# Kernel tuning notes

Measured on AMD Instinct MI355X. Metric: run time of the kernel, lower is better.

Reference implementation:

```python
import jax, jax.numpy as jnp
import numpy as np
import math

INPUT_DIM = 1024
EMBED_DIM = 1024
NUM_HEADS = 16
HEAD_DIM = EMBED_DIM // NUM_HEADS


def setup_inputs() -> dict:
    key = jax.random.key(0)
    k_x, k_qkv, k_out_w, k_out_b = jax.random.split(key, 4)
    x = jax.random.normal(k_x, (1, 4096, INPUT_DIM), dtype=jnp.float32)
    # nn.Linear weights are [out, in]; kaiming-uniform-ish scale
    s1 = 1.0 / math.sqrt(INPUT_DIM)
    s2 = 1.0 / math.sqrt(EMBED_DIM)
    qkv_w = jax.random.uniform(k_qkv, (3 * EMBED_DIM, INPUT_DIM), jnp.float32, -s1, s1)
    out_w = jax.random.uniform(k_out_w, (EMBED_DIM, EMBED_DIM), jnp.float32, -s2, s2)
    out_b = jax.random.uniform(k_out_b, (EMBED_DIM,), jnp.float32, -s2, s2)
    return {"x": x, "qkv_w": qkv_w, "out_w": out_w, "out_b": out_b}


def reference(x, qkv_w, out_w, out_b):
    B, N, C = x.shape
    qkv = jnp.einsum('bnc,ec->bne', x, qkv_w)  # [B,N,3E]
    q = qkv[:, :, 0:EMBED_DIM].reshape(B, N, NUM_HEADS, HEAD_DIM)
    k = qkv[:, :, EMBED_DIM:2 * EMBED_DIM].reshape(B, N, NUM_HEADS, HEAD_DIM)
    v = qkv[:, :, 2 * EMBED_DIM:].reshape(B, N, NUM_HEADS, HEAD_DIM)
    scores = jnp.einsum('bihd,bjhd->bhij', q, k) / jnp.sqrt(jnp.float32(HEAD_DIM))
    attn = jax.nn.softmax(scores, axis=-1)  # [B,H,N,N]
    out = jnp.einsum('bhik,bkhd->bhid', attn, v)
    out = out.transpose(0, 2, 1, 3).reshape(B, N, EMBED_DIM)
    return jnp.einsum('bne,fe->bnf', out, out_w) + out_b
```

## Files before the change

### kernel.cpp

```cpp
#include <hip/hip_runtime.h>
#include <hip/hip_bf16.h>

typedef __bf16 bf16;
typedef bf16 bf16x8 __attribute__((ext_vector_type(8)));
typedef bf16 bf16x4 __attribute__((ext_vector_type(4)));
typedef float f32x4 __attribute__((ext_vector_type(4)));

#define MFMA16(a, b, c) __builtin_amdgcn_mfma_f32_16x16x32_bf16(a, b, c, 0, 0, 0)

__device__ __forceinline__ void g2l16(const bf16* g, bf16* l) {
  __builtin_amdgcn_global_load_lds(
      (__attribute__((address_space(1))) void*)(void*)g,
      (__attribute__((address_space(3))) void*)l,
      16, 0, 0);
}

__device__ __forceinline__ int sniff_inblock(const void* x, int tid) {
  __shared__ int sf;
  if (tid < 64) {
    unsigned short v = ((const unsigned short*)x)[tid];
    int e = (v >> 7) & 0xFF;
    int sane = (e == 0) || (e >= 112 && e <= 142);
    unsigned long long m = __ballot(sane);
    if (tid == 0) sf = (__popcll(m) >= 56) ? 1 : 0;
  }
  __syncthreads();
  return sf;
}

__device__ __forceinline__ void conv8(const void* in, bf16* out, long i, int f) {
  if (f) {
    ((bf16x8*)out)[i] = ((const bf16x8*)in)[i];
  } else {
    const float4* p = (const float4*)in;
    float4 a = p[i * 2], b = p[i * 2 + 1];
    bf16x8 v;
    v[0] = (bf16)a.x; v[1] = (bf16)a.y; v[2] = (bf16)a.z; v[3] = (bf16)a.w;
    v[4] = (bf16)b.x; v[5] = (bf16)b.y; v[6] = (bf16)b.z; v[7] = (bf16)b.w;
    ((bf16x8*)out)[i] = v;
  }
}

__global__ void convert2_to_bf16(const void* __restrict__ a, bf16* __restrict__ oa,
                                 long na8, const void* __restrict__ b,
                                 bf16* __restrict__ ob, long nb8,
                                 const void* __restrict__ x) {
  const int f = sniff_inblock(x, threadIdx.x);
  long i = (long)blockIdx.x * 256 + threadIdx.x;
  if (i < na8) conv8(a, oa, i, f);
  else if (i - na8 < nb8) conv8(b, ob, i - na8, f);
}

__global__ __launch_bounds__(256) void gemm_qkv(
    const bf16* __restrict__ A, const bf16* __restrict__ B,
    bf16* __restrict__ qB, bf16* __restrict__ kP, bf16* __restrict__ vP) {
  __shared__ __align__(16) bf16 As[128 * 32];
  __shared__ __align__(16) bf16 Bs[128 * 32];

  const int tid  = threadIdx.x;
  const int lane = tid & 63;
  const int wave = tid >> 6;
  const int wm   = wave >> 1, wn = wave & 1;
  const int l15  = lane & 15, quad = lane >> 4;
  const long m0 = (long)blockIdx.x * 128;
  const long n0 = (long)blockIdx.y * 128;
  const int  K  = 1024;

  const bf16* Ab = A + m0 * K;
  const bf16* Bb = B + n0 * K;
  const int rowA = tid & 127;
  const int dc   = tid >> 7;

  f32x4 acc[4][4] = {};

  for (int k0 = 0; k0 < K; k0 += 32) {
    g2l16(Ab + (long)rowA * K + k0 + dc * 8,       As + tid * 8);
    g2l16(Ab + (long)rowA * K + k0 + (dc + 2) * 8, As + (tid + 256) * 8);
    g2l16(Bb + (long)rowA * K + k0 + dc * 8,       Bs + tid * 8);
    g2l16(Bb + (long)rowA * K + k0 + (dc + 2) * 8, Bs + (tid + 256) * 8);
    __syncthreads();

    bf16x8 af[4], bfr[4];
#pragma unroll
    for (int t = 0; t < 4; t++) {
      af[t]  = *(const bf16x8*)(As + (quad * 128 + wm * 64 + t * 16 + l15) * 8);
      bfr[t] = *(const bf16x8*)(Bs + (quad * 128 + wn * 64 + t * 16 + l15) * 8);
    }
#pragma unroll
    for (int tm = 0; tm < 4; tm++)
#pragma unroll
      for (int tn = 0; tn < 4; tn++)
        acc[tm][tn] = MFMA16(af[tm], bfr[tn], acc[tm][tn]);
    __syncthreads();
  }

  const long rb = m0 + wm * 64;
  const long cb = n0 + wn * 64;
  const int third = (int)(n0 >> 10);
  const float QSC = 0.125f * 1.44269504088896f;

#pragma unroll
  for (int tm = 0; tm < 4; tm++) {
#pragma unroll
    for (int tn = 0; tn < 4; tn++) {
      const long r0 = rb + tm * 16 + quad * 4;
      const long c  = cb + tn * 16 + l15;
      if (third == 0) {
#pragma unroll
        for (int r = 0; r < 4; r++)
          qB[(r0 + r) * 1024 + c] = (bf16)(acc[tm][tn][r] * QSC);
      } else if (third == 1) {
        const int ep = (int)c - 1024;
        const int h = ep >> 6, d = ep & 63;
        const int n0r = (int)r0;
        const int kt = n0r >> 6;
        const int kh = (n0r >> 5) & 1;
        const int t_ = (n0r >> 2) & 1;
        const int mq = (n0r >> 3) & 3;
        const long base = ((long)h * 64 + kt) * 4096 +
                          (((d >> 3) * 64) + kh * 32 + t_ * 16 + mq * 4) * 8 +
                          (d & 7);
#pragma unroll
        for (int r = 0; r < 4; r++)
          kP[base + r * 8] = (bf16)acc[tm][tn][r];
      } else {
        const int ep = (int)c - 2048;
        const int h = ep >> 6, d = ep & 63;
        const int n0r = (int)r0;
        const int kt = n0r >> 6;
        const int kh = (n0r >> 5) & 1;
        const int kq = (n0r >> 3) & 3;
        bf16x4 v;
#pragma unroll
        for (int r = 0; r < 4; r++) v[r] = (bf16)acc[tm][tn][r];
        *(bf16x4*)(vP + ((long)h * 64 + kt) * 4096 +
                   (kh * 256 + kq * 64 + d) * 8 + (quad & 1) * 4) = v;
      }
    }
  }
}

template <bool BIAS, bool DYNOUT>
__global__ __launch_bounds__(256) void gemm_bt(
    const bf16* __restrict__ A, const bf16* __restrict__ B,
    void* __restrict__ Cv, const bf16* __restrict__ bias,
    int M, int Nn, int K, const void* __restrict__ xs) {
  __shared__ __align__(16) bf16 As[128 * 32];
  __shared__ __align__(16) bf16 Bs[128 * 32];

  const int tid  = threadIdx.x;
  const int obf = DYNOUT ? sniff_inblock(xs, tid) : 1;

  const int lane = tid & 63;
  const int wave = tid >> 6;
  const int wm   = wave >> 1, wn = wave & 1;
  const int l15  = lane & 15, quad = lane >> 4;
  const long m0 = (long)blockIdx.x * 128;
  const long n0 = (long)blockIdx.y * 128;

  const bf16* Ab = A + m0 * K;
  const bf16* Bb = B + n0 * K;
  const int rowA = tid & 127;
  const int dc   = tid >> 7;

  f32x4 acc[4][4] = {};

  for (int k0 = 0; k0 < K; k0 += 32) {
    g2l16(Ab + (long)rowA * K + k0 + dc * 8,       As + tid * 8);
    g2l16(Ab + (long)rowA * K + k0 + (dc + 2) * 8, As + (tid + 256) * 8);
    g2l16(Bb + (long)rowA * K + k0 + dc * 8,       Bs + tid * 8);
    g2l16(Bb + (long)rowA * K + k0 + (dc + 2) * 8, Bs + (tid + 256) * 8);
    __syncthreads();

    bf16x8 af[4], bfr[4];
#pragma unroll
    for (int t = 0; t < 4; t++) {
      af[t]  = *(const bf16x8*)(As + (quad * 128 + wm * 64 + t * 16 + l15) * 8);
      bfr[t] = *(const bf16x8*)(Bs + (quad * 128 + wn * 64 + t * 16 + l15) * 8);
    }
#pragma unroll
    for (int tm = 0; tm < 4; tm++)
#pragma unroll
      for (int tn = 0; tn < 4; tn++)
        acc[tm][tn] = MFMA16(af[tm], bfr[tn], acc[tm][tn]);
    __syncthreads();
  }

  const long rb = m0 + wm * 64;
  const long cb = n0 + wn * 64;
#pragma unroll
  for (int tm = 0; tm < 4; tm++) {
#pragma unroll
    for (int tn = 0; tn < 4; tn++) {
      const long r0 = rb + tm * 16 + quad * 4;
      const long c  = cb + tn * 16 + l15;
      const float bv = BIAS ? (float)bias[c] : 0.0f;
#pragma unroll
      for (int r = 0; r < 4; r++) {
        const float val = acc[tm][tn][r] + bv;
        const long idx = (r0 + r) * Nn + c;
        if (DYNOUT && !obf) ((float*)Cv)[idx] = val;
        else                ((bf16*)Cv)[idx]  = (bf16)val;
      }
    }
  }
}

__global__ __launch_bounds__(128, 2) void flash_attn(
    const bf16* __restrict__ qB, const bf16* __restrict__ kP,
    const bf16* __restrict__ vP, bf16* __restrict__ O) {
  __shared__ __align__(16) bf16 KV[4][4096];
  __shared__ float lred[256];

  const int tid = threadIdx.x;
  const int lane = tid & 63;
  const int kh = tid >> 6;
  const int l15 = lane & 15, quad = lane >> 4;
  const int bid = blockIdx.x;
  const int xcd = bid & 7, bi = bid >> 3;
  const int h  = xcd + 8 * (bi >> 6);
  const int qt = bi & 63;
  const int q0 = qt * 64;

  bf16x8 qf[4][2];
#pragma unroll
  for (int g = 0; g < 4; g++) {
    const bf16* qrow = qB + (long)(q0 + g * 16 + l15) * 1024 + h * 64;
    qf[g][0] = *(const bf16x8*)(qrow + quad * 8);
    qf[g][1] = *(const bf16x8*)(qrow + 32 + quad * 8);
  }

  bf16x8 onesf;
#pragma unroll
  for (int j = 0; j < 8; j++) onesf[j] = (bf16)1.0f;

  f32x4 oa[4][4] = {};
  f32x4 la[4] = {};

  const bf16* kb = kP + (long)h * 64 * 4096;
  const bf16* vb = vP + (long)h * 64 * 4096;

#pragma unroll
  for (int i = 0; i < 4; i++) {
    g2l16(kb + (tid + i * 128) * 8, KV[0] + (tid + i * 128) * 8);
    g2l16(vb + (tid + i * 128) * 8, KV[2] + (tid + i * 128) * 8);
  }

  for (int kt = 0; kt < 64; kt++) {
    const int cur = kt & 1;
    __syncthreads();
    if (kt + 1 < 64) {
      const bf16* kn = kb + (long)(kt + 1) * 4096;
      const bf16* vn = vb + (long)(kt + 1) * 4096;
#pragma unroll
      for (int i = 0; i < 4; i++) {
        g2l16(kn + (tid + i * 128) * 8, KV[cur ^ 1] + (tid + i * 128) * 8);
        g2l16(vn + (tid + i * 128) * 8, KV[2 + (cur ^ 1)] + (tid + i * 128) * 8);
      }
    }

    const bf16* kg = KV[cur];
    const bf16* vg = KV[2 + cur];

    f32x4 s[4][2];
#pragma unroll
    for (int t = 0; t < 2; t++) {
      bf16x8 a0 = *(const bf16x8*)(kg + ((quad)*64 + kh * 32 + t * 16 + l15) * 8);
      bf16x8 a1 = *(const bf16x8*)(kg + ((4 + quad) * 64 + kh * 32 + t * 16 + l15) * 8);
      __builtin_amdgcn_s_setprio(1);
#pragma unroll
      for (int g = 0; g < 4; g++) {
        f32x4 z = {};
        z = MFMA16(a0, qf[g][0], z);
        z = MFMA16(a1, qf[g][1], z);
        s[g][t] = z;
      }
      __builtin_amdgcn_s_setprio(0);
    }

    bf16x8 pf[4];
#pragma unroll
    for (int g = 0; g < 4; g++) {
      union { bf16x8 v; __hip_bfloat162 h2[4]; } u;
#pragma unroll
      for (int idx = 0; idx < 4; idx++) {
        const int t = idx >> 1, rr = (idx & 1) * 2;
        float p0 = __builtin_amdgcn_exp2f(s[g][t][rr]);
        float p1 = __builtin_amdgcn_exp2f(s[g][t][rr + 1]);
        u.h2[idx] = __float22bfloat162_rn(float2{p0, p1});
      }
      pf[g] = u.v;
    }

#pragma unroll
    for (int dt = 0; dt < 4; dt++) {
      bf16x8 v = *(const bf16x8*)(vg + (kh * 256 + quad * 64 + dt * 16 + l15) * 8);
      __builtin_amdgcn_s_setprio(1);
#pragma unroll
      for (int g = 0; g < 4; g++) oa[g][dt] = MFMA16(v, pf[g], oa[g][dt]);
      __builtin_amdgcn_s_setprio(0);
    }
    __builtin_amdgcn_s_setprio(1);
#pragma unroll
    for (int g = 0; g < 4; g++) la[g] = MFMA16(onesf, pf[g], la[g]);
    __builtin_amdgcn_s_setprio(0);
  }

  __syncthreads();
  float* red = (float*)KV;
  if (kh == 1) {
#pragma unroll
    for (int g = 0; g < 4; g++)
#pragma unroll
      for (int dt = 0; dt < 4; dt++)
        *(f32x4*)(red + (g * 4 + dt) * 256 + lane * 4) = oa[g][dt];
#pragma unroll
    for (int g = 0; g < 4; g++) lred[g * 64 + lane] = la[g][0];
  }
  __syncthreads();
  if (kh == 0) {
#pragma unroll
    for (int g = 0; g < 4; g++) {
#pragma unroll
      for (int dt = 0; dt < 4; dt++)
        oa[g][dt] += *(const f32x4*)(red + (g * 4 + dt) * 256 + lane * 4);
      const float l = la[g][0] + lred[g * 64 + lane];
      const float inv = 1.0f / l;
      bf16* orow = O + (long)(q0 + g * 16 + l15) * 1024 + h * 64;
#pragma unroll
      for (int dt = 0; dt < 4; dt++) {
        bf16x4 v;
#pragma unroll
        for (int r = 0; r < 4; r++) v[r] = (bf16)(oa[g][dt][r] * inv);
        *(bf16x4*)(orow + dt * 16 + quad * 4) = v;
      }
    }
  }
}

extern "C" void kernel_launch(void* const* d_in, const int* in_sizes, int n_in,
                              void* d_out, int out_size, void* d_ws, size_t ws_size,
                              hipStream_t stream) {
  const void* x     = d_in[0];
  const void* qkv_w = d_in[1];
  const void* out_w = d_in[2];
  const void* out_b = d_in[3];

  char* ws = (char*)d_ws;
  bf16* qB   = (bf16*)(ws);
  bf16* kP   = (bf16*)(ws + 8388608);
  bf16* vP   = (bf16*)(ws + 16777216);
  bf16* ob   = (bf16*)(ws + 25165824);
  bf16* qwb  = (bf16*)(ws + 33554432);
  bf16* xb   = ob;
  bf16* owb  = qB;
  bf16* obb  = qB + 1048576;

  convert2_to_bf16<<<3584, 256, 0, stream>>>(x, xb, 524288, qkv_w, qwb, 393216, x);

  gemm_qkv<<<dim3(32, 24), 256, 0, stream>>>(xb, qwb, qB, kP, vP);

  flash_attn<<<1024, 128, 0, stream>>>(qB, kP, vP, ob);

  convert2_to_bf16<<<513, 256, 0, stream>>>(out_w, owb, 131072, out_b, obb, 128, x);

  gemm_bt<true, true><<<dim3(32, 8), 256, 0, stream>>>(
      ob, owb, d_out, obb, 4096, 1024, 1024, x);
}
```

Baseline: 249.6 us.

## Load K/V directly from global into registers, dropping LDS staging and barriers

```diff
diff --git a/kernel.cpp b/kernel.cpp
--- a/kernel.cpp
+++ b/kernel.cpp
@@ -206,10 +206,68 @@
   }
 }
 
+__device__ __forceinline__ void attn_tile(
+    int kt, const bf16* kb, const bf16* vb, int quad, int koff, int voff,
+    const bf16x8 (&qf)[4][2], const bf16x8 (&kcur)[2][2], bf16x8 (&knxt)[2][2],
+    const bf16x8& onesf, f32x4 (&oa)[4][4], f32x4 (&la)[4]) {
+  bf16x8 vf[4];
+  const bf16* vt = vb + (long)kt * 4096;
+#pragma unroll
+  for (int dt = 0; dt < 4; dt++)
+    vf[dt] = *(const bf16x8*)(vt + dt * 128 + voff);
+
+  f32x4 s[4][2];
+#pragma unroll
+  for (int t = 0; t < 2; t++) {
+    __builtin_amdgcn_s_setprio(1);
+#pragma unroll
+    for (int g = 0; g < 4; g++) {
+      f32x4 z = {};
+      z = MFMA16(kcur[t][0], qf[g][0], z);
+      z = MFMA16(kcur[t][1], qf[g][1], z);
+      s[g][t] = z;
+    }
+    __builtin_amdgcn_s_setprio(0);
+  }
+
+  const bf16* kn = kb + (long)(kt + 1) * 4096;
+#pragma unroll
+  for (int t = 0; t < 2; t++)
+#pragma unroll
+    for (int j = 0; j < 2; j++)
+      knxt[t][j] = *(const bf16x8*)(kn + (j * 4 + quad) * 512 + t * 128 + koff);
+
+  bf16x8 pf[4];
+#pragma unroll
+  for (int g = 0; g < 4; g++) {
+    union { bf16x8 v; __hip_bfloat162 h2[4]; } u;
+#pragma unroll
+    for (int idx = 0; idx < 4; idx++) {
+      const int t = idx >> 1, rr = (idx & 1) * 2;
+      float p0 = __builtin_amdgcn_exp2f(s[g][t][rr]);
+      float p1 = __builtin_amdgcn_exp2f(s[g][t][rr + 1]);
+      u.h2[idx] = __float22bfloat162_rn(float2{p0, p1});
+    }
+    pf[g] = u.v;
+  }
+
+#pragma unroll
+  for (int dt = 0; dt < 4; dt++) {
+    __builtin_amdgcn_s_setprio(1);
+#pragma unroll
+    for (int g = 0; g < 4; g++) oa[g][dt] = MFMA16(vf[dt], pf[g], oa[g][dt]);
+    __builtin_amdgcn_s_setprio(0);
+  }
+  __builtin_amdgcn_s_setprio(1);
+#pragma unroll
+  for (int g = 0; g < 4; g++) la[g] = MFMA16(onesf, pf[g], la[g]);
+  __builtin_amdgcn_s_setprio(0);
+}
+
 __global__ __launch_bounds__(128, 2) void flash_attn(
     const bf16* __restrict__ qB, const bf16* __restrict__ kP,
     const bf16* __restrict__ vP, bf16* __restrict__ O) {
-  __shared__ __align__(16) bf16 KV[4][4096];
+  __shared__ __align__(16) float red[4096];
   __shared__ float lred[256];
 
   const int tid = threadIdx.x;
@@ -240,74 +298,22 @@
   const bf16* kb = kP + (long)h * 64 * 4096;
   const bf16* vb = vP + (long)h * 64 * 4096;
 
-#pragma unroll
-  for (int i = 0; i < 4; i++) {
-    g2l16(kb + (tid + i * 128) * 8, KV[0] + (tid + i * 128) * 8);
-    g2l16(vb + (tid + i * 128) * 8, KV[2] + (tid + i * 128) * 8);
-  }
-
-  for (int kt = 0; kt < 64; kt++) {
-    const int cur = kt & 1;
-    __syncthreads();
-    if (kt + 1 < 64) {
-      const bf16* kn = kb + (long)(kt + 1) * 4096;
-      const bf16* vn = vb + (long)(kt + 1) * 4096;
-#pragma unroll
-      for (int i = 0; i < 4; i++) {
-        g2l16(kn + (tid + i * 128) * 8, KV[cur ^ 1] + (tid + i * 128) * 8);
-        g2l16(vn + (tid + i * 128) * 8, KV[2 + (cur ^ 1)] + (tid + i * 128) * 8);
-      }
-    }
-
-    const bf16* kg = KV[cur];
-    const bf16* vg = KV[2 + cur];
-
-    f32x4 s[4][2];
-#pragma unroll
-    for (int t = 0; t < 2; t++) {
-      bf16x8 a0 = *(const bf16x8*)(kg + ((quad)*64 + kh * 32 + t * 16 + l15) * 8);
-      bf16x8 a1 = *(const bf16x8*)(kg + ((4 + quad) * 64 + kh * 32 + t * 16 + l15) * 8);
-      __builtin_amdgcn_s_setprio(1);
-#pragma unroll
-      for (int g = 0; g < 4; g++) {
-        f32x4 z = {};
-        z = MFMA16(a0, qf[g][0], z);
-        z = MFMA16(a1, qf[g][1], z);
-        s[g][t] = z;
-      }
-      __builtin_amdgcn_s_setprio(0);
-    }
-
-    bf16x8 pf[4];
-#pragma unroll
-    for (int g = 0; g < 4; g++) {
-      union { bf16x8 v; __hip_bfloat162 h2[4]; } u;
-#pragma unroll
-      for (int idx = 0; idx < 4; idx++) {
-        const int t = idx >> 1, rr = (idx & 1) * 2;
-        float p0 = __builtin_amdgcn_exp2f(s[g][t][rr]);
-        float p1 = __builtin_amdgcn_exp2f(s[g][t][rr + 1]);
-        u.h2[idx] = __float22bfloat162_rn(float2{p0, p1});
-      }
-      pf[g] = u.v;
-    }
-
-#pragma unroll
-    for (int dt = 0; dt < 4; dt++) {
-      bf16x8 v = *(const bf16x8*)(vg + (kh * 256 + quad * 64 + dt * 16 + l15) * 8);
-      __builtin_amdgcn_s_setprio(1);
-#pragma unroll
-      for (int g = 0; g < 4; g++) oa[g][dt] = MFMA16(v, pf[g], oa[g][dt]);
-      __builtin_amdgcn_s_setprio(0);
-    }
-    __builtin_amdgcn_s_setprio(1);
-#pragma unroll
-    for (int g = 0; g < 4; g++) la[g] = MFMA16(onesf, pf[g], la[g]);
-    __builtin_amdgcn_s_setprio(0);
-  }
-
-  __syncthreads();
-  float* red = (float*)KV;
+  const int koff = (kh * 32 + l15) * 8;
+  const int voff = (kh * 256 + quad * 64 + l15) * 8;
+
+  bf16x8 kA[2][2], kB[2][2];
+#pragma unroll
+  for (int t = 0; t < 2; t++)
+#pragma unroll
+    for (int j = 0; j < 2; j++)
+      kA[t][j] = *(const bf16x8*)(kb + (j * 4 + quad) * 512 + t * 128 + koff);
+
+#pragma unroll 1
+  for (int kt = 0; kt < 64; kt += 2) {
+    attn_tile(kt,     kb, vb, quad, koff, voff, qf, kA, kB, onesf, oa, la);
+    attn_tile(kt + 1, kb, vb, quad, koff, voff, qf, kB, kA, onesf, oa, la);
+  }
+
   if (kh == 1) {
 #pragma unroll
     for (int g = 0; g < 4; g++)
```

New measurement: 233.5 us. 1.07x faster.
